# Performance work log

Hardware: AMD Instinct MI355X
Metric: run time of the kernel (lower is better)

The kernel has to match this reference:

```python
import jax, jax.numpy as jnp
import numpy as np

EPS = 1e-5  # torch InstanceNorm2d default eps


def setup_inputs() -> dict:
    key = jax.random.key(0)
    k1, k2, k3, k4 = jax.random.split(key, 4)
    B, C, H, W = 32, 256, 64, 64
    S = 16
    x = jax.random.normal(k1, (B, C, H, W), dtype=jnp.float32)
    style_id = jax.random.randint(k2, (B,), 0, S, dtype=jnp.int64)
    gamma = jax.random.normal(k3, (S, C), dtype=jnp.float32)
    beta = jax.random.normal(k4, (S, C), dtype=jnp.float32)
    return {"x": x, "style_id": style_id, "gamma": gamma, "beta": beta}


def reference(x, style_id, gamma, beta):
    # Per-sample, per-channel instance norm over spatial dims (biased var),
    # with style-indexed affine params (torch InstanceNorm2d, affine=True).
    mean = jnp.mean(x, axis=(2, 3), keepdims=True)          # [B,C,1,1]
    var = jnp.mean(jnp.square(x - mean), axis=(2, 3), keepdims=True)
    x_hat = (x - mean) * jax.lax.rsqrt(var + EPS)
    g = gamma[style_id][:, :, None, None]                   # [B,C,1,1]
    b = beta[style_id][:, :, None, None]
    return x_hat * g + b
```

## Files before the change

### kernel.cpp

```cpp
#include <hip/hip_runtime.h>


#define HW   4096
#define NC   256
#define NTHR 64

typedef float vfloat4 __attribute__((ext_vector_type(4)));

__global__ __launch_bounds__(NTHR) void cin2d_kernel(
    const float* __restrict__ x,
    const int* __restrict__ style_id,
    const float* __restrict__ gamma,
    const float* __restrict__ beta,
    float* __restrict__ out)
{
    const int lane = threadIdx.x;
    const int inst = blockIdx.x;
    const int b = inst >> 8;
    const int c = inst & (NC - 1);

    const vfloat4* xp = (const vfloat4*)(x + (size_t)inst * HW) + lane;

    vfloat4 d[16];
#pragma unroll
    for (int i = 0; i < 16; ++i) d[i] = xp[i * 64];

#pragma unroll
    for (int i = 0; i < 16; ++i) {
        asm volatile("" : "+v"(d[i]));
    }

    const int sid = style_id[b];
    const float g  = gamma[sid * NC + c];
    const float be = beta[sid * NC + c];

    float s0 = 0.f, s1 = 0.f, s2 = 0.f, s3 = 0.f;
    float q0 = 0.f, q1 = 0.f, q2 = 0.f, q3 = 0.f;
#pragma unroll
    for (int i = 0; i < 16; ++i) {
        s0 += d[i][0];  q0 = fmaf(d[i][0], d[i][0], q0);
        s1 += d[i][1];  q1 = fmaf(d[i][1], d[i][1], q1);
        s2 += d[i][2];  q2 = fmaf(d[i][2], d[i][2], q2);
        s3 += d[i][3];  q3 = fmaf(d[i][3], d[i][3], q3);
    }
    float s = (s0 + s1) + (s2 + s3);
    float q = (q0 + q1) + (q2 + q3);

#pragma unroll
    for (int off = 1; off < 64; off <<= 1) {
        s += __shfl_xor(s, off, 64);
        q += __shfl_xor(q, off, 64);
    }

    const float inv_n = 1.0f / (float)HW;
    const float mean = s * inv_n;
    float var = fmaf(-mean, mean, q * inv_n);
    var = var < 0.0f ? 0.0f : var;
    const float rstd = rsqrtf(var + 1e-5f);

    const float scale = g * rstd;
    const float shift = fmaf(-mean, scale, be);

    vfloat4* op = (vfloat4*)(out + (size_t)inst * HW) + lane;
#pragma unroll
    for (int i = 0; i < 16; ++i) {
        vfloat4 w;
#pragma unroll
        for (int j = 0; j < 4; ++j) w[j] = fmaf(d[i][j], scale, shift);
        op[i * 64] = w;
    }
}

extern "C" void kernel_launch(void* const* d_in, const int* in_sizes, int n_in,
                              void* d_out, int out_size, void* d_ws, size_t ws_size,
                              hipStream_t stream) {
    const float* x     = (const float*)d_in[0];
    const int*   sid   = (const int*)d_in[1];
    const float* gamma = (const float*)d_in[2];
    const float* beta  = (const float*)d_in[3];
    float* out = (float*)d_out;

    const int B = 32, C = 256;
    dim3 grid(B * C), block(NTHR);
    hipLaunchKernelGGL(cin2d_kernel, grid, block, 0, stream,
                       x, sid, gamma, beta, out);
}
```

Baseline: 234.7 us.

## Process four instances per wave with register double-buffered prefetch and nontemporal stores

Each 64-thread wave now normalizes four consecutive (batch, channel) instances, loading the next instance's data into a second register buffer while reducing and writing the current one. Output writes use nontemporal stores to avoid polluting caches. The grid shrinks from 8192 to 2048 waves, trading wave-level parallelism for explicit in-wave load/compute overlap and higher register use.

```diff
diff --git a/kernel.cpp b/kernel.cpp
--- a/kernel.cpp
+++ b/kernel.cpp
@@ -1,74 +1,90 @@
 #include <hip/hip_runtime.h>
 
 
-#define HW   4096
-#define NC   256
-#define NTHR 64
+#define HW    4096
+#define NC    256
+#define NPER  4
+#define NWAVE 2048
 
 typedef float vfloat4 __attribute__((ext_vector_type(4)));
 
-__global__ __launch_bounds__(NTHR) void cin2d_kernel(
+__global__ __launch_bounds__(64, 2) void cin2d_kernel(
     const float* __restrict__ x,
     const int* __restrict__ style_id,
     const float* __restrict__ gamma,
     const float* __restrict__ beta,
     float* __restrict__ out)
 {
-    const int lane = threadIdx.x;
-    const int inst = blockIdx.x;
-    const int b = inst >> 8;
-    const int c = inst & (NC - 1);
+    const int lane  = threadIdx.x;
+    const int inst0 = blockIdx.x * NPER;
 
-    const vfloat4* xp = (const vfloat4*)(x + (size_t)inst * HW) + lane;
+    const vfloat4* xp = (const vfloat4*)(x   + (size_t)inst0 * HW) + lane;
+    vfloat4*       op = (vfloat4*)      (out + (size_t)inst0 * HW) + lane;
 
-    vfloat4 d[16];
-#pragma unroll
-    for (int i = 0; i < 16; ++i) d[i] = xp[i * 64];
+    vfloat4 A[16], B[16];
 
 #pragma unroll
-    for (int i = 0; i < 16; ++i) {
-        asm volatile("" : "+v"(d[i]));
-    }
+    for (int i = 0; i < 16; ++i) A[i] = xp[i * 64];
 
-    const int sid = style_id[b];
-    const float g  = gamma[sid * NC + c];
-    const float be = beta[sid * NC + c];
+    auto STEP = [&](vfloat4 (&CUR)[16], vfloat4 (&NXT)[16], int k,
+                    bool prefetch) {
+        if (prefetch) {
+            const vfloat4* xn = xp + (size_t)(k + 1) * (HW / 4);
+#pragma unroll
+            for (int i = 0; i < 16; ++i) NXT[i] = xn[i * 64];
+        }
 
-    float s0 = 0.f, s1 = 0.f, s2 = 0.f, s3 = 0.f;
-    float q0 = 0.f, q1 = 0.f, q2 = 0.f, q3 = 0.f;
-#pragma unroll
-    for (int i = 0; i < 16; ++i) {
-        s0 += d[i][0];  q0 = fmaf(d[i][0], d[i][0], q0);
-        s1 += d[i][1];  q1 = fmaf(d[i][1], d[i][1], q1);
-        s2 += d[i][2];  q2 = fmaf(d[i][2], d[i][2], q2);
-        s3 += d[i][3];  q3 = fmaf(d[i][3], d[i][3], q3);
-    }
-    float s = (s0 + s1) + (s2 + s3);
-    float q = (q0 + q1) + (q2 + q3);
+        const int inst = inst0 + k;
+        const int b = inst >> 8;
+        const int c = inst & (NC - 1);
+        const int sid = style_id[b];
+        const float g  = gamma[sid * NC + c];
+        const float be = beta[sid * NC + c];
 
 #pragma unroll
-    for (int off = 1; off < 64; off <<= 1) {
-        s += __shfl_xor(s, off, 64);
-        q += __shfl_xor(q, off, 64);
-    }
+        for (int i = 0; i < 16; ++i) asm volatile("" : "+v"(CUR[i]));
 
-    const float inv_n = 1.0f / (float)HW;
-    const float mean = s * inv_n;
-    float var = fmaf(-mean, mean, q * inv_n);
-    var = var < 0.0f ? 0.0f : var;
-    const float rstd = rsqrtf(var + 1e-5f);
+        float s0 = 0.f, s1 = 0.f, s2 = 0.f, s3 = 0.f;
+        float q0 = 0.f, q1 = 0.f, q2 = 0.f, q3 = 0.f;
+#pragma unroll
+        for (int i = 0; i < 16; ++i) {
+            s0 += CUR[i][0];  q0 = fmaf(CUR[i][0], CUR[i][0], q0);
+            s1 += CUR[i][1];  q1 = fmaf(CUR[i][1], CUR[i][1], q1);
+            s2 += CUR[i][2];  q2 = fmaf(CUR[i][2], CUR[i][2], q2);
+            s3 += CUR[i][3];  q3 = fmaf(CUR[i][3], CUR[i][3], q3);
+        }
+        float s = (s0 + s1) + (s2 + s3);
+        float q = (q0 + q1) + (q2 + q3);
 
-    const float scale = g * rstd;
-    const float shift = fmaf(-mean, scale, be);
+#pragma unroll
+        for (int off = 1; off < 64; off <<= 1) {
+            s += __shfl_xor(s, off, 64);
+            q += __shfl_xor(q, off, 64);
+        }
 
-    vfloat4* op = (vfloat4*)(out + (size_t)inst * HW) + lane;
+        const float inv_n = 1.0f / (float)HW;
+        const float mean = s * inv_n;
+        float var = fmaf(-mean, mean, q * inv_n);
+        var = var < 0.0f ? 0.0f : var;
+        const float rstd = rsqrtf(var + 1e-5f);
+
+        const float scale = g * rstd;
+        const float shift = fmaf(-mean, scale, be);
+
+        vfloat4* o = op + (size_t)k * (HW / 4);
 #pragma unroll
-    for (int i = 0; i < 16; ++i) {
-        vfloat4 w;
+        for (int i = 0; i < 16; ++i) {
+            vfloat4 w;
 #pragma unroll
-        for (int j = 0; j < 4; ++j) w[j] = fmaf(d[i][j], scale, shift);
-        op[i * 64] = w;
-    }
+            for (int j = 0; j < 4; ++j) w[j] = fmaf(CUR[i][j], scale, shift);
+            __builtin_nontemporal_store(w, &o[i * 64]);
+        }
+    };
+
+    STEP(A, B, 0, true);
+    STEP(B, A, 1, true);
+    STEP(A, B, 2, true);
+    STEP(B, A, 3, false);
 }
 
 extern "C" void kernel_launch(void* const* d_in, const int* in_sizes, int n_in,
@@ -80,8 +96,7 @@
     const float* beta  = (const float*)d_in[3];
     float* out = (float*)d_out;
 
-    const int B = 32, C = 256;
-    dim3 grid(B * C), block(NTHR);
+    dim3 grid(NWAVE), block(64);
     hipLaunchKernelGGL(cin2d_kernel, grid, block, 0, stream,
                        x, sid, gamma, beta, out);
 }
```

After: 240.8 us. 1.03x slower.
